# Optimization experiments

Hardware: AMD Instinct MI355X
Metric: run time of the kernel (lower is better)

Reference implementation:

```python
import jax, jax.numpy as jnp
import numpy as np

B, WK, HRS = 2048, 52, 8760
DT = 0.125          # Euler step in days (3-hourly), exactly representable
RANGE_PRED = 7      # forecast horizon in days


def setup_inputs() -> dict:
    key = jax.random.key(0)
    k1, k2, k3, k4 = jax.random.split(key, 4)
    # X_in: [B, weeks, 5, 1]; channel 0 = start time in days (same across batch,
    # the torch code reads X_in[0, week, 0, 0]); channels 1..4 = N,P,Z,D init.
    X_in = jax.random.uniform(k1, (B, WK, 5, 1), jnp.float32, 0.1, 3.0)
    t0 = jnp.arange(WK, dtype=jnp.float32) * 7.0
    X_in = X_in.at[:, :, 0, 0].set(jnp.broadcast_to(t0, (B, WK)))
    global_f = jax.random.uniform(k2, (B, HRS), jnp.float32)          # light forcing in [0,1]
    global_m = jax.random.uniform(k3, (B, HRS), jnp.float32) * 0.1    # mixing rate, small
    params_value = jax.random.uniform(k4, (B, 10), jnp.float32, 0.1, 1.0)
    return {"X_in": X_in, "global_f": global_f, "global_m": global_m,
            "params_value": params_value, "dt": DT, "range_pred": RANGE_PRED}


def reference(X_in, global_f, global_m, params_value, dt, range_pred):
    # Fixed multipliers from the torch code
    pv = jnp.asarray([1.0, 2.0, 0.1, 0.05, 0.1, 0.3, 0.6, 0.15, 0.4, 0.1], X_in.dtype)
    Q0, Vm, thr = 8.0, 1.0, 0.01  # Q0 = 4 + 2.5 + 1.5 + 0
    chi, rho, gam, lam, eps, alp, bet, eta, phi, zet = [params_value[:, i][:, None] for i in range(10)]  # [B,1]

    n_steps = int(round(range_pred / dt))      # 56
    stride = int(round(1.0 / dt))              # 8 -> daily sampling of output

    # Hourly forcing gather: same time axis for every batch element (torch uses X_in[0,...])
    t0 = X_in[0, :, 0, 0]                                                     # [W]
    times = t0[:, None] + jnp.arange(n_steps + 1, dtype=X_in.dtype) * dt      # [W, S]
    idx = jnp.round(times * 24.0).astype(jnp.int32)
    f = jnp.take(global_f, idx, axis=1)[:, :, :n_steps]                       # [B, W, T]
    m = jnp.take(global_m, idx, axis=1)[:, :, :n_steps]

    def step(carry, ft_mt):
        N, P, Z, D = carry                      # each [B, W]
        ft, mt = ft_mt
        Pc = jnp.maximum(thr, P)
        Zc = jnp.maximum(thr, Z)
        gN = N / (chi * pv[0] + N)
        zg = rho * pv[1] * (1.0 - jnp.exp(-lam * pv[3] * Pc)) * Zc
        up = Vm * gN * ft * Pc
        Nn = N + dt * (-up + alp * pv[5] * zg + eps * pv[4] * P + gam * pv[2] * Z + phi * pv[8] * D + mt * (Q0 - N))
        Pn = P + dt * (up - zg - eps * pv[4] * P - eta * pv[7] * P - mt * P)
        Zn = Z + dt * (bet * pv[6] * zg - gam * pv[2] * Z - mt * Z)
        Dn = D + dt * (eta * pv[7] * P + (1.0 - alp * pv[5] - bet * pv[6]) * zg - phi * pv[8] * D - zet * pv[9] * D - mt * D)
        new = (Nn, Pn, Zn, Dn)
        return new, jnp.stack(new, axis=0)      # [4, B, W]

    carry0 = (X_in[:, :, 1, 0], X_in[:, :, 2, 0], X_in[:, :, 3, 0], X_in[:, :, 4, 0])
    _, ys = jax.lax.scan(step, carry0, (jnp.moveaxis(f, 2, 0), jnp.moveaxis(m, 2, 0)))  # ys: [T, 4, B, W]
    traj = jnp.concatenate([jnp.stack(carry0, axis=0)[None], ys], axis=0)               # [S, 4, B, W]
    out = jnp.moveaxis(traj, (0, 1), (3, 2))                                            # [B, W, 4, S]
    return out[:, :, :, ::stride]               # daily samples: [B, W, 4, range_pred+1]
```

## Files before the change

### kernel.cpp

```cpp
#include <hip/hip_runtime.h>
#include <hip/hip_bf16.h>


typedef float f32x4 __attribute__((ext_vector_type(4)));

#define NPZD_B 2048
#define NPZD_WK 52
#define NPZD_HRS 8760
#define NPZD_NSTEPS 56
#define NPZD_NF4 2190
#define NPZD_WSTRIDE 60
#define NPZD_LDSW (NPZD_WK * NPZD_WSTRIDE + 16)

__global__ __launch_bounds__(256) void npzd_kernel(
    const float* __restrict__ X_in,
    const float* __restrict__ gf,
    const float* __restrict__ gm,
    const float* __restrict__ params,
    const float* __restrict__ dt_ptr,
    float* __restrict__ out)
{
    __shared__ __align__(16) float lds_f[NPZD_LDSW];
    __shared__ __align__(16) float lds_m[NPZD_LDSW];

    const int b   = blockIdx.x;
    const int tid = threadIdx.x;

    const f32x4* __restrict__ gf4 = (const f32x4*)(gf + (size_t)b * NPZD_HRS);
    const f32x4* __restrict__ gm4 = (const f32x4*)(gm + (size_t)b * NPZD_HRS);

    f32x4 fv[9], mv[9];
    int kk[9];
    #pragma unroll
    for (int i = 0; i < 9; ++i) {
        int k = i * 256 + tid;
        if (k >= NPZD_NF4) k = NPZD_NF4 - 1;
        kk[i] = k;
        fv[i] = __builtin_nontemporal_load(gf4 + k);
        mv[i] = __builtin_nontemporal_load(gm4 + k);
    }

    #pragma unroll
    for (int i = 0; i < 9; ++i) {
        const int k = kk[i];
        const float fe[4] = {fv[i].x, fv[i].y, fv[i].z, fv[i].w};
        const float me[4] = {mv[i].x, mv[i].y, mv[i].z, mv[i].w};
        const int rm = k % 3;
        const int e0 = (rm == 0) ? 0 : (3 - rm);
        const int j0 = (4 * k + e0) / 3;
        const int p0 = j0 + 4 * ((j0 * 9363) >> 19);
        lds_f[p0] = fe[e0];
        lds_m[p0] = me[e0];
        if (rm == 0) {
            const int j1 = j0 + 1;
            const int p1 = j1 + 4 * ((j1 * 9363) >> 19);
            lds_f[p1] = fe[3];
            lds_m[p1] = me[3];
        }
    }
    __syncthreads();

    if (tid >= NPZD_WK) return;
    const int w = tid;

    const float dt = dt_ptr[0];

    const float* xb = X_in + ((size_t)b * NPZD_WK + w) * 5;
    float N = xb[1], P = xb[2], Z = xb[3], D = xb[4];

    const float* pp = params + (size_t)b * 10;
    const float chi   = pp[0];
    const float rho2  = pp[1] * 2.0f;
    const float gam1  = pp[2] * 0.1f;
    const float lam05 = pp[3] * 0.05f;
    const float eps1  = pp[4] * 0.1f;
    const float alp3  = pp[5] * 0.3f;
    const float bet6  = pp[6] * 0.6f;
    const float eta15 = pp[7] * 0.15f;
    const float phi4  = pp[8] * 0.4f;
    const float zet1  = pp[9] * 0.1f;
    const float rem   = 1.0f - alp3 - bet6;

    float oN[8], oP[8], oZ[8], oD[8];
    oN[0] = N; oP[0] = P; oZ[0] = Z; oD[0] = D;

    const float* lf = lds_f + w * NPZD_WSTRIDE;
    const float* lm = lds_m + w * NPZD_WSTRIDE;

    #pragma unroll
    for (int g = 0; g < 14; ++g) {
        const f32x4 f4 = *(const f32x4*)(lf + 4 * g);
        const f32x4 m4 = *(const f32x4*)(lm + 4 * g);
        const float fs[4] = {f4.x, f4.y, f4.z, f4.w};
        const float ms[4] = {m4.x, m4.y, m4.z, m4.w};
        #pragma unroll
        for (int q = 0; q < 4; ++q) {
            const float ft = fs[q], mt = ms[q];
            const float Pc = fmaxf(0.01f, P);
            const float Zc = fmaxf(0.01f, Z);
            const float gN = N * __builtin_amdgcn_rcpf(chi + N);
            const float zg = rho2 * (1.0f - __expf(-lam05 * Pc)) * Zc;
            const float up = gN * ft * Pc;
            const float Nn = N + dt * (-up + alp3 * zg + eps1 * P + gam1 * Z + phi4 * D + mt * (8.0f - N));
            const float Pn = P + dt * (up - zg - eps1 * P - eta15 * P - mt * P);
            const float Zn = Z + dt * (bet6 * zg - gam1 * Z - mt * Z);
            const float Dn = D + dt * (eta15 * P + rem * zg - phi4 * D - zet1 * D - mt * D);
            N = Nn; P = Pn; Z = Zn; D = Dn;
        }
        if (g & 1) {
            const int c = (g >> 1) + 1;
            oN[c] = N; oP[c] = P; oZ[c] = Z; oD[c] = D;
        }
    }

    f32x4* o4 = (f32x4*)(out + ((size_t)b * NPZD_WK + w) * 32);
    o4[0] = (f32x4){oN[0], oN[1], oN[2], oN[3]};
    o4[1] = (f32x4){oN[4], oN[5], oN[6], oN[7]};
    o4[2] = (f32x4){oP[0], oP[1], oP[2], oP[3]};
    o4[3] = (f32x4){oP[4], oP[5], oP[6], oP[7]};
    o4[4] = (f32x4){oZ[0], oZ[1], oZ[2], oZ[3]};
    o4[5] = (f32x4){oZ[4], oZ[5], oZ[6], oZ[7]};
    o4[6] = (f32x4){oD[0], oD[1], oD[2], oD[3]};
    o4[7] = (f32x4){oD[4], oD[5], oD[6], oD[7]};
}

extern "C" void kernel_launch(void* const* d_in, const int* in_sizes, int n_in,
                              void* d_out, int out_size, void* d_ws, size_t ws_size,
                              hipStream_t stream) {
    const float* X_in   = (const float*)d_in[0];
    const float* gf     = (const float*)d_in[1];
    const float* gm     = (const float*)d_in[2];
    const float* params = (const float*)d_in[3];
    const float* dt_ptr = (const float*)d_in[4];
    float* out = (float*)d_out;

    npzd_kernel<<<NPZD_B, 256, 0, stream>>>(X_in, gf, gm, params, dt_ptr, out);
}
```

Baseline: 170.9 us.

## Split each batch row across two blocks, each handling half the weeks

Launches two blocks per batch element instead of one. Each block loads only the half of the forcing arrays its 26 weeks need into a half-sized LDS buffer, then integrates those weeks. This doubles the grid, halves per-block load work and LDS use, and should raise occupancy and memory-latency hiding. The cost is more blocks with even fewer active compute threads each, plus duplicated parameter setup per block.

```diff
diff --git a/kernel.cpp b/kernel.cpp
--- a/kernel.cpp
+++ b/kernel.cpp
@@ -7,10 +7,10 @@
 #define NPZD_B 2048
 #define NPZD_WK 52
 #define NPZD_HRS 8760
-#define NPZD_NSTEPS 56
-#define NPZD_NF4 2190
+#define NPZD_HWK 26
+#define NPZD_NF4H 1092
 #define NPZD_WSTRIDE 60
-#define NPZD_LDSW (NPZD_WK * NPZD_WSTRIDE + 16)
+#define NPZD_LDSW (NPZD_HWK * NPZD_WSTRIDE + 16)
 
 __global__ __launch_bounds__(256) void npzd_kernel(
     const float* __restrict__ X_in,
@@ -23,45 +23,50 @@
     __shared__ __align__(16) float lds_f[NPZD_LDSW];
     __shared__ __align__(16) float lds_m[NPZD_LDSW];
 
-    const int b   = blockIdx.x;
+    const int blk = blockIdx.x;
+    const int b   = blk >> 1;
+    const int q   = blk & 1;
     const int tid = threadIdx.x;
 
     const f32x4* __restrict__ gf4 = (const f32x4*)(gf + (size_t)b * NPZD_HRS);
     const f32x4* __restrict__ gm4 = (const f32x4*)(gm + (size_t)b * NPZD_HRS);
 
-    f32x4 fv[9], mv[9];
-    int kk[9];
+    const int k0   = q * NPZD_NF4H;
+    const int kmax = k0 + NPZD_NF4H - 1;
+    f32x4 fv[5], mv[5];
+    int kk[5];
     #pragma unroll
-    for (int i = 0; i < 9; ++i) {
-        int k = i * 256 + tid;
-        if (k >= NPZD_NF4) k = NPZD_NF4 - 1;
+    for (int i = 0; i < 5; ++i) {
+        int k = k0 + i * 256 + tid;
+        if (k > kmax) k = kmax;
         kk[i] = k;
         fv[i] = __builtin_nontemporal_load(gf4 + k);
         mv[i] = __builtin_nontemporal_load(gm4 + k);
     }
 
+    const int pbase = 1560 * q;
     #pragma unroll
-    for (int i = 0; i < 9; ++i) {
+    for (int i = 0; i < 5; ++i) {
         const int k = kk[i];
         const float fe[4] = {fv[i].x, fv[i].y, fv[i].z, fv[i].w};
         const float me[4] = {mv[i].x, mv[i].y, mv[i].z, mv[i].w};
         const int rm = k % 3;
         const int e0 = (rm == 0) ? 0 : (3 - rm);
         const int j0 = (4 * k + e0) / 3;
-        const int p0 = j0 + 4 * ((j0 * 9363) >> 19);
+        const int p0 = j0 + 4 * ((j0 * 9363) >> 19) - pbase;
         lds_f[p0] = fe[e0];
         lds_m[p0] = me[e0];
         if (rm == 0) {
             const int j1 = j0 + 1;
-            const int p1 = j1 + 4 * ((j1 * 9363) >> 19);
+            const int p1 = j1 + 4 * ((j1 * 9363) >> 19) - pbase;
             lds_f[p1] = fe[3];
             lds_m[p1] = me[3];
         }
     }
     __syncthreads();
 
-    if (tid >= NPZD_WK) return;
-    const int w = tid;
+    if (tid >= NPZD_HWK) return;
+    const int w = q * NPZD_HWK + tid;
 
     const float dt = dt_ptr[0];
 
@@ -84,8 +89,8 @@
     float oN[8], oP[8], oZ[8], oD[8];
     oN[0] = N; oP[0] = P; oZ[0] = Z; oD[0] = D;
 
-    const float* lf = lds_f + w * NPZD_WSTRIDE;
-    const float* lm = lds_m + w * NPZD_WSTRIDE;
+    const float* lf = lds_f + tid * NPZD_WSTRIDE;
+    const float* lm = lds_m + tid * NPZD_WSTRIDE;
 
     #pragma unroll
     for (int g = 0; g < 14; ++g) {
@@ -94,8 +99,8 @@
         const float fs[4] = {f4.x, f4.y, f4.z, f4.w};
         const float ms[4] = {m4.x, m4.y, m4.z, m4.w};
         #pragma unroll
-        for (int q = 0; q < 4; ++q) {
-            const float ft = fs[q], mt = ms[q];
+        for (int qq = 0; qq < 4; ++qq) {
+            const float ft = fs[qq], mt = ms[qq];
             const float Pc = fmaxf(0.01f, P);
             const float Zc = fmaxf(0.01f, Z);
             const float gN = N * __builtin_amdgcn_rcpf(chi + N);
@@ -134,5 +139,5 @@
     const float* dt_ptr = (const float*)d_in[4];
     float* out = (float*)d_out;
 
-    npzd_kernel<<<NPZD_B, 256, 0, stream>>>(X_in, gf, gm, params, dt_ptr, out);
+    npzd_kernel<<<NPZD_B * 2, 256, 0, stream>>>(X_in, gf, gm, params, dt_ptr, out);
 }
```

Result: slower. 175.8 us (+2.8%).
